# Kernel optimization log

Measured on AMD Instinct MI355X. Metric: run time of the kernel, lower is better.

Reference implementation:

```python
import jax, jax.numpy as jnp
import numpy as np

NUM_SEGMENTS = 100000


def setup_inputs() -> dict:
    key = jax.random.key(0)
    k1, k2 = jax.random.split(key)
    x = jax.random.normal(k1, (4000000, 32), dtype=jnp.float32)
    index = jax.random.randint(k2, (4000000,), 0, NUM_SEGMENTS, dtype=jnp.int64)
    return {"x": x, "index": index}


def reference(x, index):
    # scatter_mean(x, index, dim=0): sum rows per segment, divide by count (clamped to 1)
    sums = jax.ops.segment_sum(x, index, num_segments=NUM_SEGMENTS)  # [S, D]
    counts = jax.ops.segment_sum(jnp.ones((x.shape[0],), dtype=x.dtype), index,
                                 num_segments=NUM_SEGMENTS)  # [S]
    return sums / jnp.maximum(counts, 1.0)[:, None]
```

## Files before the change

### kernel.cpp

```cpp
#include <hip/hip_runtime.h>

#define NSEG 100000
#define DIM 32
#define SCAN_BLOCK 1024

__global__ void hist_kernel(const int* __restrict__ idx, int* __restrict__ cnt, int n) {
    int i = blockIdx.x * blockDim.x + threadIdx.x;
    if (i < n) atomicAdd(&cnt[idx[i]], 1);
}

__global__ void scan_block_reduce(const int* __restrict__ cnt, int* __restrict__ bsums, int nseg) {
    __shared__ int lds[SCAN_BLOCK];
    int i = blockIdx.x * SCAN_BLOCK + threadIdx.x;
    lds[threadIdx.x] = (i < nseg) ? cnt[i] : 0;
    __syncthreads();
    for (int off = SCAN_BLOCK / 2; off > 0; off >>= 1) {
        if (threadIdx.x < off) lds[threadIdx.x] += lds[threadIdx.x + off];
        __syncthreads();
    }
    if (threadIdx.x == 0) bsums[blockIdx.x] = lds[0];
}

__global__ void scan_bsums(int* __restrict__ bsums, int nb) {
    __shared__ int lds[128];
    int t = threadIdx.x;
    int v = (t < nb) ? bsums[t] : 0;
    lds[t] = v;
    __syncthreads();
    for (int off = 1; off < 128; off <<= 1) {
        int add = (t >= off) ? lds[t - off] : 0;
        __syncthreads();
        lds[t] += add;
        __syncthreads();
    }
    if (t < nb) bsums[t] = lds[t] - v;
}

__global__ void scan_final(const int* __restrict__ cnt, const int* __restrict__ bsums,
                           int* __restrict__ offs, int* __restrict__ cursor, int nseg) {
    __shared__ int lds[SCAN_BLOCK];
    int t = threadIdx.x;
    int i = blockIdx.x * SCAN_BLOCK + t;
    int v = (i < nseg) ? cnt[i] : 0;
    lds[t] = v;
    __syncthreads();
    for (int off = 1; off < SCAN_BLOCK; off <<= 1) {
        int add = (t >= off) ? lds[t - off] : 0;
        __syncthreads();
        lds[t] += add;
        __syncthreads();
    }
    if (i < nseg) {
        int e = bsums[blockIdx.x] + lds[t] - v;
        offs[i] = e;
        cursor[i] = e;
    }
}

__global__ void scatter_ids(const int* __restrict__ idx, int* __restrict__ cursor,
                            int* __restrict__ rowid, int n) {
    int i = blockIdx.x * blockDim.x + threadIdx.x;
    if (i < n) {
        int pos = atomicAdd(&cursor[idx[i]], 1);
        rowid[pos] = i;
    }
}

__global__ void seg_sum(const float* __restrict__ x, const int* __restrict__ rowid,
                        const int* __restrict__ offs, const int* __restrict__ cnt,
                        float* __restrict__ out, int nseg) {
    int wave = threadIdx.x >> 6;
    int lane = threadIdx.x & 63;
    int seg = blockIdx.x * (blockDim.x >> 6) + wave;
    if (seg >= nseg) return;
    int start = offs[seg];
    int count = cnt[seg];
    int col = lane & 31;
    int slot = lane >> 5;
    float acc = 0.f;
    for (int j = start + slot; j < start + count; j += 2) {
        int r = rowid[j];
        acc += x[(size_t)r * DIM + col];
    }
    acc += __shfl_down(acc, 32, 64);
    if (slot == 0) {
        out[(size_t)seg * DIM + col] = acc / fmaxf((float)count, 1.0f);
    }
}

__global__ void scatter_sum_kernel(const float* __restrict__ x,
                                   const int* __restrict__ idx,
                                   float* __restrict__ sums,
                                   float* __restrict__ cnts,
                                   int n_elems) {
    int i = blockIdx.x * blockDim.x + threadIdx.x;
    if (i >= n_elems) return;
    int row = i >> 5;
    int col = i & 31;
    int seg = idx[row];
    atomicAdd(&sums[seg * DIM + col], x[i]);
    if (col == 0) atomicAdd(&cnts[seg], 1.0f);
}

__global__ void divide_kernel(float* __restrict__ out, const float* __restrict__ cnts, int n) {
    int i = blockIdx.x * blockDim.x + threadIdx.x;
    if (i >= n) return;
    float c = cnts[i >> 5];
    out[i] = out[i] / fmaxf(c, 1.0f);
}

extern "C" void kernel_launch(void* const* d_in, const int* in_sizes, int n_in,
                              void* d_out, int out_size, void* d_ws, size_t ws_size,
                              hipStream_t stream) {
    const float* x   = (const float*)d_in[0];
    const int*   idx = (const int*)d_in[1];
    float* out = (float*)d_out;

    int N = in_sizes[1];
    int n_elems = in_sizes[0];

    const int nb_scan = (NSEG + SCAN_BLOCK - 1) / SCAN_BLOCK;
    size_t needed = (size_t)(3 * NSEG + 128 + N) * sizeof(int);

    if (ws_size < needed) {
        float* cnts = (float*)d_ws;
        hipMemsetAsync(d_out, 0, (size_t)out_size * sizeof(float), stream);
        hipMemsetAsync(d_ws, 0, (size_t)NSEG * sizeof(float), stream);
        int blocks = (n_elems + 255) / 256;
        scatter_sum_kernel<<<blocks, 256, 0, stream>>>(x, idx, out, cnts, n_elems);
        divide_kernel<<<(out_size + 255) / 256, 256, 0, stream>>>(out, cnts, out_size);
        return;
    }

    int* cnt    = (int*)d_ws;
    int* offs   = cnt + NSEG;
    int* cursor = offs + NSEG;
    int* bsums  = cursor + NSEG;
    int* rowid  = bsums + 128;

    hipMemsetAsync(cnt, 0, (size_t)NSEG * sizeof(int), stream);

    hist_kernel<<<(N + 255) / 256, 256, 0, stream>>>(idx, cnt, N);
    scan_block_reduce<<<nb_scan, SCAN_BLOCK, 0, stream>>>(cnt, bsums, NSEG);
    scan_bsums<<<1, 128, 0, stream>>>(bsums, nb_scan);
    scan_final<<<nb_scan, SCAN_BLOCK, 0, stream>>>(cnt, bsums, offs, cursor, NSEG);
    scatter_ids<<<(N + 255) / 256, 256, 0, stream>>>(idx, cursor, rowid, N);

    int segblocks = (NSEG + 3) / 4;
    seg_sum<<<segblocks, 256, 0, stream>>>(x, rowid, offs, cnt, out, NSEG);
}
```

Before: 1.365 ms.

## Replace per-segment sort with coarse bucket partition and LDS accumulation

Segments are grouped into 500 buckets of 200. A per-block LDS histogram builds a bucket-by-block count matrix, which is scanned. A partition pass then writes packed (local segment, row) entries using LDS cursors. Each bucket block accumulates its rows into shared-memory accumulators with LDS atomics and writes the means. This removes the global atomics on 100k counters and the separate per-segment offset arrays. The cost is lower grid parallelism in the sum stage (500 blocks), LDS atomic contention, and a 24-bit limit on row ids in the packed format.

```diff
diff --git a/kernel.cpp b/kernel.cpp
--- a/kernel.cpp
+++ b/kernel.cpp
@@ -2,17 +2,30 @@
 
 #define NSEG 100000
 #define DIM 32
+#define SPB 200
+#define NBUCKET 500
+#define NPBLK 250
 #define SCAN_BLOCK 1024
+#define SUM_THREADS 512
 
-__global__ void hist_kernel(const int* __restrict__ idx, int* __restrict__ cnt, int n) {
-    int i = blockIdx.x * blockDim.x + threadIdx.x;
-    if (i < n) atomicAdd(&cnt[idx[i]], 1);
+__global__ void count_matrix(const int* __restrict__ idx, int* __restrict__ cntmat,
+                             int N, int chunk) {
+    __shared__ int lh[NBUCKET];
+    for (int t = threadIdx.x; t < NBUCKET; t += blockDim.x) lh[t] = 0;
+    __syncthreads();
+    int lo = blockIdx.x * chunk;
+    int hi = min(lo + chunk, N);
+    for (int i = lo + threadIdx.x; i < hi; i += blockDim.x)
+        atomicAdd(&lh[idx[i] / SPB], 1);
+    __syncthreads();
+    for (int t = threadIdx.x; t < NBUCKET; t += blockDim.x)
+        cntmat[t * NPBLK + blockIdx.x] = lh[t];
 }
 
-__global__ void scan_block_reduce(const int* __restrict__ cnt, int* __restrict__ bsums, int nseg) {
+__global__ void scan_block_reduce(const int* __restrict__ v, int* __restrict__ bsums, int M) {
     __shared__ int lds[SCAN_BLOCK];
     int i = blockIdx.x * SCAN_BLOCK + threadIdx.x;
-    lds[threadIdx.x] = (i < nseg) ? cnt[i] : 0;
+    lds[threadIdx.x] = (i < M) ? v[i] : 0;
     __syncthreads();
     for (int off = SCAN_BLOCK / 2; off > 0; off >>= 1) {
         if (threadIdx.x < off) lds[threadIdx.x] += lds[threadIdx.x + off];
@@ -36,13 +49,12 @@
     if (t < nb) bsums[t] = lds[t] - v;
 }
 
-__global__ void scan_final(const int* __restrict__ cnt, const int* __restrict__ bsums,
-                           int* __restrict__ offs, int* __restrict__ cursor, int nseg) {
+__global__ void scan_final_inplace(int* __restrict__ v, const int* __restrict__ bsums, int M) {
     __shared__ int lds[SCAN_BLOCK];
     int t = threadIdx.x;
     int i = blockIdx.x * SCAN_BLOCK + t;
-    int v = (i < nseg) ? cnt[i] : 0;
-    lds[t] = v;
+    int val = (i < M) ? v[i] : 0;
+    lds[t] = val;
     __syncthreads();
     for (int off = 1; off < SCAN_BLOCK; off <<= 1) {
         int add = (t >= off) ? lds[t - off] : 0;
@@ -50,41 +62,65 @@
         lds[t] += add;
         __syncthreads();
     }
-    if (i < nseg) {
-        int e = bsums[blockIdx.x] + lds[t] - v;
-        offs[i] = e;
-        cursor[i] = e;
+    if (i < M) v[i] = bsums[blockIdx.x] + lds[t] - val;
+}
+
+__global__ void partition_rows(const int* __restrict__ idx, const int* __restrict__ scan,
+                               int* __restrict__ packed, int N, int chunk) {
+    __shared__ int lcur[NBUCKET];
+    for (int t = threadIdx.x; t < NBUCKET; t += blockDim.x)
+        lcur[t] = scan[t * NPBLK + blockIdx.x];
+    __syncthreads();
+    int lo = blockIdx.x * chunk;
+    int hi = min(lo + chunk, N);
+    for (int i = lo + threadIdx.x; i < hi; i += blockDim.x) {
+        int s = idx[i];
+        int b = s / SPB;
+        int ls = s - b * SPB;
+        int pos = atomicAdd(&lcur[b], 1);
+        packed[pos] = (ls << 24) | i;
     }
 }
 
-__global__ void scatter_ids(const int* __restrict__ idx, int* __restrict__ cursor,
-                            int* __restrict__ rowid, int n) {
-    int i = blockIdx.x * blockDim.x + threadIdx.x;
-    if (i < n) {
-        int pos = atomicAdd(&cursor[idx[i]], 1);
-        rowid[pos] = i;
+__global__ void __launch_bounds__(SUM_THREADS)
+bucket_sum(const float* __restrict__ x, const int* __restrict__ packed,
+           const int* __restrict__ scan, float* __restrict__ out, int N) {
+    __shared__ float acc[SPB * DIM];
+    __shared__ int cl[SPB];
+    for (int t = threadIdx.x; t < SPB * DIM; t += SUM_THREADS) acc[t] = 0.f;
+    for (int t = threadIdx.x; t < SPB; t += SUM_THREADS) cl[t] = 0;
+    __syncthreads();
+
+    int b = blockIdx.x;
+    int start = scan[b * NPBLK];
+    int end = (b == NBUCKET - 1) ? N : scan[(b + 1) * NPBLK];
+
+    int wid  = threadIdx.x >> 6;
+    int lane = threadIdx.x & 63;
+    int slot = lane >> 5;
+    int col  = lane & 31;
+
+    for (int base = start; base < end; base += 64) {
+#pragma unroll
+        for (int k = 0; k < 4; ++k) {
+            int j = base + wid * 8 + k * 2 + slot;
+            if (j < end) {
+                int p = packed[j];
+                int row = p & 0xFFFFFF;
+                int ls = ((unsigned)p) >> 24;
+                float v = x[(size_t)row * DIM + col];
+                atomicAdd(&acc[ls * DIM + col], v);
+                if (col == 0) atomicAdd(&cl[ls], 1);
+            }
+        }
     }
-}
+    __syncthreads();
 
-__global__ void seg_sum(const float* __restrict__ x, const int* __restrict__ rowid,
-                        const int* __restrict__ offs, const int* __restrict__ cnt,
-                        float* __restrict__ out, int nseg) {
-    int wave = threadIdx.x >> 6;
-    int lane = threadIdx.x & 63;
-    int seg = blockIdx.x * (blockDim.x >> 6) + wave;
-    if (seg >= nseg) return;
-    int start = offs[seg];
-    int count = cnt[seg];
-    int col = lane & 31;
-    int slot = lane >> 5;
-    float acc = 0.f;
-    for (int j = start + slot; j < start + count; j += 2) {
-        int r = rowid[j];
-        acc += x[(size_t)r * DIM + col];
-    }
-    acc += __shfl_down(acc, 32, 64);
-    if (slot == 0) {
-        out[(size_t)seg * DIM + col] = acc / fmaxf((float)count, 1.0f);
+    for (int t = threadIdx.x; t < SPB * DIM; t += SUM_THREADS) {
+        int ls = t >> 5;
+        int seg = b * SPB + ls;
+        if (seg < NSEG)
+            out[(size_t)seg * DIM + (t & 31)] = acc[t] / fmaxf((float)cl[ls], 1.0f);
     }
 }
 
@@ -119,8 +155,9 @@
     int N = in_sizes[1];
     int n_elems = in_sizes[0];
 
-    const int nb_scan = (NSEG + SCAN_BLOCK - 1) / SCAN_BLOCK;
-    size_t needed = (size_t)(3 * NSEG + 128 + N) * sizeof(int);
+    const int M = NBUCKET * NPBLK;
+    const int nb_scan = (M + SCAN_BLOCK - 1) / SCAN_BLOCK;
+    size_t needed = ((size_t)M + 128 + (size_t)N) * sizeof(int);
 
     if (ws_size < needed) {
         float* cnts = (float*)d_ws;
@@ -132,20 +169,16 @@
         return;
     }
 
-    int* cnt    = (int*)d_ws;
-    int* offs   = cnt + NSEG;
-    int* cursor = offs + NSEG;
-    int* bsums  = cursor + NSEG;
-    int* rowid  = bsums + 128;
+    int* cntmat = (int*)d_ws;
+    int* bsums  = cntmat + M;
+    int* packed = bsums + 128;
 
-    hipMemsetAsync(cnt, 0, (size_t)NSEG * sizeof(int), stream);
+    int chunk = (N + NPBLK - 1) / NPBLK;
 
-    hist_kernel<<<(N + 255) / 256, 256, 0, stream>>>(idx, cnt, N);
-    scan_block_reduce<<<nb_scan, SCAN_BLOCK, 0, stream>>>(cnt, bsums, NSEG);
+    count_matrix<<<NPBLK, 256, 0, stream>>>(idx, cntmat, N, chunk);
+    scan_block_reduce<<<nb_scan, SCAN_BLOCK, 0, stream>>>(cntmat, bsums, M);
     scan_bsums<<<1, 128, 0, stream>>>(bsums, nb_scan);
-    scan_final<<<nb_scan, SCAN_BLOCK, 0, stream>>>(cnt, bsums, offs, cursor, NSEG);
-    scatter_ids<<<(N + 255) / 256, 256, 0, stream>>>(idx, cursor, rowid, N);
-
-    int segblocks = (NSEG + 3) / 4;
-    seg_sum<<<segblocks, 256, 0, stream>>>(x, rowid, offs, cnt, out, NSEG);
+    scan_final_inplace<<<nb_scan, SCAN_BLOCK, 0, stream>>>(cntmat, bsums, M);
+    partition_rows<<<NPBLK, 256, 0, stream>>>(idx, cntmat, packed, N, chunk);
+    bucket_sum<<<NBUCKET, SUM_THREADS, 0, stream>>>(x, packed, cntmat, out, N);
 }
```

Result: faster. 1.336 ms (-2.1%).
